# Kernel tuning notes

Measured on AMD Instinct MI355X. Metric: run time of the kernel, lower is better.

The kernel has to match this reference:

```python
import jax, jax.numpy as jnp
import numpy as np

EMBED_DIM = 1024
N_HEADS = 16
HEAD_DIM = EMBED_DIM // N_HEADS
SEQ_LEN = 4096


def setup_inputs() -> dict:
    key = jax.random.key(0)
    k1, k2 = jax.random.split(key)
    x = jax.random.normal(k1, (SEQ_LEN, EMBED_DIM), dtype=jnp.float32)
    # Linear params (lecun-normal-ish scale)
    W_qkv = jax.random.normal(k2, (EMBED_DIM, 3 * EMBED_DIM), dtype=jnp.float32) / np.sqrt(EMBED_DIM)
    b_qkv = jnp.zeros((3 * EMBED_DIM,), dtype=jnp.float32)
    return {"x": x, "W_qkv": W_qkv, "b_qkv": b_qkv}


def reference(x, W_qkv, b_qkv):
    T = x.shape[0]
    # Fused QKV projection: [T, 3*E]
    qkv = x @ W_qkv + b_qkv
    q, k, v = jnp.split(qkv, 3, axis=-1)
    # [T, N, H]
    q = q.reshape(T, N_HEADS, HEAD_DIM)
    k = k.reshape(T, N_HEADS, HEAD_DIM)
    v = v.reshape(T, N_HEADS, HEAD_DIM)
    # Standard SDPA (module does NOT pass is_causal, so full attention)
    scale = 1.0 / np.sqrt(HEAD_DIM).astype(np.float32)
    logits = jnp.einsum("qnh,knh->nqk", q, k) * scale  # [N, T, T]
    attn = jax.nn.softmax(logits, axis=-1)
    y = jnp.einsum("nqk,knh->qnh", attn, v)  # [T, N, H]
    return y
```

## Files before the change

### kernel.cpp

```cpp
#include <hip/hip_runtime.h>

#define T_SEQ 4096
#define EMB   1024
#define NH    16
#define HD    64
#define N3    3072

#define SCL2 0.18033688011112042f

using u16 = unsigned short;
using u32 = unsigned int;
typedef __bf16 bf16x8 __attribute__((ext_vector_type(8)));
typedef float  f32x4  __attribute__((ext_vector_type(4)));
typedef float  f32x16 __attribute__((ext_vector_type(16)));
typedef u16    u16x8  __attribute__((ext_vector_type(8)));

#if __has_builtin(__builtin_amdgcn_exp2f)
#define EXP2(x) __builtin_amdgcn_exp2f(x)
#else
#define EXP2(x) exp2f(x)
#endif

__device__ inline u16 f2bf(float f) {
    union { float f; unsigned u; } v; v.f = f;
    unsigned u = v.u;
    u += 0x7FFFu + ((u >> 16) & 1u);
    return (u16)(u >> 16);
}

__global__ void convert_x_kernel(const float* __restrict__ x, u16* __restrict__ xb) {
    int i = (blockIdx.x * 256 + threadIdx.x) * 8;
    float4 a = *(const float4*)(x + i);
    float4 b = *(const float4*)(x + i + 4);
    u16x8 o;
    o[0] = f2bf(a.x); o[1] = f2bf(a.y); o[2] = f2bf(a.z); o[3] = f2bf(a.w);
    o[4] = f2bf(b.x); o[5] = f2bf(b.y); o[6] = f2bf(b.z); o[7] = f2bf(b.w);
    *(u16x8*)(xb + i) = o;
}

__global__ void transpose_w_kernel(const float* __restrict__ W, u16* __restrict__ Wt) {
    __shared__ float tile[64][72];
    int n0 = blockIdx.x * 64, k0 = blockIdx.y * 64;
    float qs = (n0 < 1024) ? SCL2 : 1.0f;
    int t = threadIdx.x;
#pragma unroll
    for (int p = 0; p < 16; ++p) {
        int idx = p * 256 + t;
        int r = idx >> 6, c = idx & 63;
        tile[r][c] = W[(k0 + r) * N3 + n0 + c];
    }
    __syncthreads();
    int c2 = t >> 2;
    int kg = (t & 3) * 16;
    u16x8 o0, o1;
#pragma unroll
    for (int j = 0; j < 8; ++j) o0[j] = f2bf(tile[kg + j][c2] * qs);
#pragma unroll
    for (int j = 0; j < 8; ++j) o1[j] = f2bf(tile[kg + 8 + j][c2] * qs);
    u16* dst = Wt + (n0 + c2) * EMB + k0 + kg;
    *(u16x8*)dst = o0;
    *(u16x8*)(dst + 8) = o1;
}

__global__ __launch_bounds__(256) void gemm_qkv_kernel(const u16* __restrict__ xb,
                                                       const u16* __restrict__ Wt,
                                                       const float* __restrict__ bias,
                                                       u16* __restrict__ qkv) {
    __shared__ __align__(16) u16 Alds[128 * 64];
    __shared__ __align__(16) u16 Blds[128 * 64];
    int tid = threadIdx.x;
    int lane = tid & 63, wave = tid >> 6;
    int wm = wave >> 1, wn = wave & 1;
    int m0 = blockIdx.y * 128, n0 = blockIdx.x * 128;
    int lr = lane & 15, lg = lane >> 4;

    f32x4 acc[4][4] = {};

    for (int kt = 0; kt < 16; ++kt) {
        int kbase = kt * 64;
#pragma unroll
        for (int p = 0; p < 4; ++p) {
            int g = p * 256 + tid;
            int row = g >> 3;
            int cg = (g & 7) << 3;
            int sg = (((cg >> 3) ^ (row & 7)) << 3);
            u16x8 va = *(const u16x8*)(xb + (m0 + row) * EMB + kbase + cg);
            *(u16x8*)&Alds[row * 64 + sg] = va;
            u16x8 vb = *(const u16x8*)(Wt + (n0 + row) * EMB + kbase + cg);
            *(u16x8*)&Blds[row * 64 + sg] = vb;
        }
        __syncthreads();
#pragma unroll
        for (int ks = 0; ks < 2; ++ks) {
            bf16x8 af[4], bf[4];
#pragma unroll
            for (int mi = 0; mi < 4; ++mi) {
                int row = wm * 64 + mi * 16 + lr;
                int sg = ((ks * 4 + lg) ^ (row & 7)) << 3;
                af[mi] = *(const bf16x8*)&Alds[row * 64 + sg];
            }
#pragma unroll
            for (int ni = 0; ni < 4; ++ni) {
                int row = wn * 64 + ni * 16 + lr;
                int sg = ((ks * 4 + lg) ^ (row & 7)) << 3;
                bf[ni] = *(const bf16x8*)&Blds[row * 64 + sg];
            }
#pragma unroll
            for (int mi = 0; mi < 4; ++mi)
#pragma unroll
                for (int ni = 0; ni < 4; ++ni)
                    acc[mi][ni] = __builtin_amdgcn_mfma_f32_16x16x32_bf16(af[mi], bf[ni], acc[mi][ni], 0, 0, 0);
        }
        __syncthreads();
    }
#pragma unroll
    for (int ni = 0; ni < 4; ++ni) {
        int n = n0 + wn * 64 + ni * 16 + lr;
        float bv = bias[n];
        if (n < 1024) bv *= SCL2;
#pragma unroll
        for (int mi = 0; mi < 4; ++mi) {
            int mrow = m0 + wm * 64 + mi * 16 + lg * 4;
#pragma unroll
            for (int r = 0; r < 4; ++r)
                qkv[(mrow + r) * N3 + n] = f2bf(acc[mi][ni][r] + bv);
        }
    }
}

__global__ void transpose_v_kernel(const u16* __restrict__ qkv, u16* __restrict__ Vt) {
    __shared__ u16 tile[64][72];
    int c0 = blockIdx.x * 64;
    int t0 = blockIdx.y * 64;
    int t = threadIdx.x;
#pragma unroll
    for (int p = 0; p < 16; ++p) {
        int idx = p * 256 + t;
        int r = idx >> 6, c = idx & 63;
        tile[r][c] = qkv[(t0 + r) * N3 + 2048 + c0 + c];
    }
    __syncthreads();
    int c2 = t >> 2;
    int kg = (t & 3) * 16;
    u16x8 o0, o1;
#pragma unroll
    for (int j = 0; j < 8; ++j) o0[j] = tile[kg + j][c2];
#pragma unroll
    for (int j = 0; j < 8; ++j) o1[j] = tile[kg + 8 + j][c2];
    u16* dst = Vt + (c0 + c2) * T_SEQ + t0 + kg;
    *(u16x8*)dst = o0;
    *(u16x8*)(dst + 8) = o1;
}

__device__ inline u32 cvtpk(float lo, float hi) {
    u32 r;
    asm("v_cvt_pk_bf16_f32 %0, %1, %2" : "=v"(r) : "v"(lo), "v"(hi));
    return r;
}

__device__ inline bf16x8 mk8(u32 w0, u32 w1, u32 w2, u32 w3) {
    union { u32 w[4]; bf16x8 v; } u;
    u.w[0] = w0; u.w[1] = w1; u.w[2] = w2; u.w[3] = w3;
    return u.v;
}

__device__ inline float vsum16(f32x16 v) {
    float a0 = v[0] + v[1],  a1 = v[2] + v[3];
    float a2 = v[4] + v[5],  a3 = v[6] + v[7];
    float a4 = v[8] + v[9],  a5 = v[10] + v[11];
    float a6 = v[12] + v[13], a7 = v[14] + v[15];
    float b0 = a0 + a1, b1 = a2 + a3, b2 = a4 + a5, b3 = a6 + a7;
    return (b0 + b1) + (b2 + b3);
}

__device__ inline void pack2(f32x16 p, int hi, bf16x8& fe, bf16x8& fo) {
    u32 a0 = cvtpk(p[0], p[1]),   a1 = cvtpk(p[2], p[3]);
    u32 a2 = cvtpk(p[4], p[5]),   a3 = cvtpk(p[6], p[7]);
    u32 b0 = cvtpk(p[8], p[9]),   b1 = cvtpk(p[10], p[11]);
    u32 b2 = cvtpk(p[12], p[13]), b3 = cvtpk(p[14], p[15]);
    u32 xa0 = (u32)__shfl_xor((int)a0, 32), xa1 = (u32)__shfl_xor((int)a1, 32);
    u32 xa2 = (u32)__shfl_xor((int)a2, 32), xa3 = (u32)__shfl_xor((int)a3, 32);
    u32 xb0 = (u32)__shfl_xor((int)b0, 32), xb1 = (u32)__shfl_xor((int)b1, 32);
    u32 xb2 = (u32)__shfl_xor((int)b2, 32), xb3 = (u32)__shfl_xor((int)b3, 32);
    fe = hi ? mk8(xa2, xa3, a2, a3) : mk8(a0, a1, xa0, xa1);
    fo = hi ? mk8(xb2, xb3, b2, b3) : mk8(b0, b1, xb0, xb1);
}

#define KVROW 72

__global__ __launch_bounds__(512, 4) void attn_kernel(const u16* __restrict__ qkv,
                                                      const u16* __restrict__ Vt,
                                                      float* __restrict__ out) {
    __shared__ __align__(16) char smem[73728];

    int tid = threadIdx.x, lane = tid & 63, wave = tid >> 6;
    int ql = lane & 31, hi = lane >> 5;
    int g = tid >> 8;
    int wq = wave & 3;
    int tid2 = tid & 255;
    int h = blockIdx.y;
    int q0 = blockIdx.x * 128;

    char* base = smem + g * 36864;
    u16* K0 = (u16*)base;
    u16* V0 = (u16*)(base + 9216);
    u16* K1 = (u16*)(base + 18432);
    u16* V1 = (u16*)(base + 27648);

    bf16x8 qf[4];
    {
        const u16* qp = qkv + (size_t)(q0 + wq * 32 + ql) * N3 + h * HD;
#pragma unroll
        for (int c = 0; c < 4; ++c)
            qf[c] = *(const bf16x8*)(qp + c * 16 + hi * 8);
    }

    f32x16 acc0 = {}, acc1 = {};
    float lrun = 0.f;

    int srow0 = tid2 >> 3, spg = tid2 & 7;
    int srow1 = srow0 + 32;
    const u16* kptr = qkv + (size_t)(g * 2048) * N3 + EMB + h * HD;
    const u16* vptr = Vt + (size_t)(h * HD) * T_SEQ + g * 2048;
    int woff0 = srow0 * KVROW + spg * 8;
    int woff1 = srow1 * KVROW + spg * 8;

    u16x8 kst0 = *(const u16x8*)(kptr + (size_t)srow0 * N3 + spg * 8);
    u16x8 kst1 = *(const u16x8*)(kptr + (size_t)srow1 * N3 + spg * 8);
    u16x8 vst0 = *(const u16x8*)(vptr + (size_t)srow0 * T_SEQ + spg * 8);
    u16x8 vst1 = *(const u16x8*)(vptr + (size_t)srow1 * T_SEQ + spg * 8);

    int koff = ql * KVROW + hi * 8;

    for (int t = 0; t < 32; ++t) {
        u16* Kl = (t & 1) ? K1 : K0;
        u16* Vl = (t & 1) ? V1 : V0;
        *(u16x8*)&Kl[woff0] = kst0;
        *(u16x8*)&Kl[woff1] = kst1;
        *(u16x8*)&Vl[woff0] = vst0;
        *(u16x8*)&Vl[woff1] = vst1;
        if (t < 31) {
            const u16* kb = kptr + (size_t)(t + 1) * 64 * N3;
            const u16* vb = vptr + (t + 1) * 64;
            kst0 = *(const u16x8*)(kb + (size_t)srow0 * N3 + spg * 8);
            kst1 = *(const u16x8*)(kb + (size_t)srow1 * N3 + spg * 8);
            vst0 = *(const u16x8*)(vb + (size_t)srow0 * T_SEQ + spg * 8);
            vst1 = *(const u16x8*)(vb + (size_t)srow1 * T_SEQ + spg * 8);
        }
        __syncthreads();

        f32x16 s0 = {}, s1 = {};
#pragma unroll
        for (int c = 0; c < 4; ++c) {
            bf16x8 kf = *(const bf16x8*)&Kl[koff + c * 16];
            s0 = __builtin_amdgcn_mfma_f32_32x32x16_bf16(kf, qf[c], s0, 0, 0, 0);
        }
#pragma unroll
        for (int c = 0; c < 4; ++c) {
            bf16x8 kf = *(const bf16x8*)&Kl[koff + 32 * KVROW + c * 16];
            s1 = __builtin_amdgcn_mfma_f32_32x32x16_bf16(kf, qf[c], s1, 0, 0, 0);
        }

#pragma unroll
        for (int r = 0; r < 16; ++r) s0[r] = EXP2(s0[r]);
#pragma unroll
        for (int r = 0; r < 16; ++r) s1[r] = EXP2(s1[r]);

        {
            float ss = vsum16(s0) + vsum16(s1);
            ss += __shfl_xor(ss, 32);
            lrun += ss;
        }

        bf16x8 pa0, pa1, pa2, pa3;
        pack2(s0, hi, pa0, pa1);
        pack2(s1, hi, pa2, pa3);

#pragma unroll
        for (int c = 0; c < 4; ++c) {
            bf16x8 pb = (c == 0) ? pa0 : (c == 1) ? pa1 : (c == 2) ? pa2 : pa3;
            bf16x8 vf0 = *(const bf16x8*)&Vl[koff + c * 16];
            acc0 = __builtin_amdgcn_mfma_f32_32x32x16_bf16(vf0, pb, acc0, 0, 0, 0);
            bf16x8 vf1 = *(const bf16x8*)&Vl[koff + 32 * KVROW + c * 16];
            acc1 = __builtin_amdgcn_mfma_f32_32x32x16_bf16(vf1, pb, acc1, 0, 0, 0);
        }
    }

    __syncthreads();

    float* Xb = (float*)(smem + 36864);
    float* lX = Xb + 4 * 32 * 68;

    if (g == 1) {
        float* ob = Xb + wq * (32 * 68);
#pragma unroll
        for (int gg = 0; gg < 4; ++gg) {
            f32x4 w0 = { acc0[4 * gg], acc0[4 * gg + 1], acc0[4 * gg + 2], acc0[4 * gg + 3] };
            *(f32x4*)&ob[ql * 68 + 8 * gg + 4 * hi] = w0;
            f32x4 w1 = { acc1[4 * gg], acc1[4 * gg + 1], acc1[4 * gg + 2], acc1[4 * gg + 3] };
            *(f32x4*)&ob[ql * 68 + 32 + 8 * gg + 4 * hi] = w1;
        }
        if (hi == 0) lX[wq * 32 + ql] = lrun;
    }
    __syncthreads();

    if (g == 0) {
        float* ob = Xb + wq * (32 * 68);
        float inv = 1.0f / (lrun + lX[wq * 32 + ql]);
        float* tb = (float*)smem + wq * (32 * 68);
#pragma unroll
        for (int gg = 0; gg < 4; ++gg) {
            f32x4 x0 = *(const f32x4*)&ob[ql * 68 + 8 * gg + 4 * hi];
            f32x4 w0 = { (acc0[4 * gg] + x0[0]) * inv, (acc0[4 * gg + 1] + x0[1]) * inv,
                         (acc0[4 * gg + 2] + x0[2]) * inv, (acc0[4 * gg + 3] + x0[3]) * inv };
            *(f32x4*)&tb[ql * 68 + 8 * gg + 4 * hi] = w0;
            f32x4 x1 = *(const f32x4*)&ob[ql * 68 + 32 + 8 * gg + 4 * hi];
            f32x4 w1 = { (acc1[4 * gg] + x1[0]) * inv, (acc1[4 * gg + 1] + x1[1]) * inv,
                         (acc1[4 * gg + 2] + x1[2]) * inv, (acc1[4 * gg + 3] + x1[3]) * inv };
            *(f32x4*)&tb[ql * 68 + 32 + 8 * gg + 4 * hi] = w1;
        }
    }
    __syncthreads();

    if (g == 0) {
        float* tb = (float*)smem + wq * (32 * 68);
#pragma unroll
        for (int qq = 0; qq < 8; ++qq) {
            int q = qq * 4 + (lane >> 4);
            int d4 = (lane & 15) * 4;
            f32x4 v = *(const f32x4*)&tb[q * 68 + d4];
            *(f32x4*)&out[(size_t)(q0 + wq * 32 + q) * EMB + h * HD + d4] = v;
        }
    }
}

extern "C" void kernel_launch(void* const* d_in, const int* in_sizes, int n_in,
                              void* d_out, int out_size, void* d_ws, size_t ws_size,
                              hipStream_t stream) {
    (void)in_sizes; (void)n_in; (void)out_size; (void)ws_size;
    const float* x = (const float*)d_in[0];
    const float* W = (const float*)d_in[1];
    const float* b = (const float*)d_in[2];
    float* out = (float*)d_out;

    u16* xb  = (u16*)d_ws;
    u16* Wt  = xb  + (size_t)T_SEQ * EMB;
    u16* qkv = Wt  + (size_t)N3 * EMB;
    u16* Vt  = qkv + (size_t)T_SEQ * N3;

    convert_x_kernel<<<(T_SEQ * EMB) / (256 * 8), 256, 0, stream>>>(x, xb);
    transpose_w_kernel<<<dim3(N3 / 64, EMB / 64), 256, 0, stream>>>(W, Wt);
    gemm_qkv_kernel<<<dim3(N3 / 128, T_SEQ / 128), 256, 0, stream>>>(xb, Wt, b, qkv);
    transpose_v_kernel<<<dim3(EMB / 64, T_SEQ / 64), 256, 0, stream>>>(qkv, Vt);
    attn_kernel<<<dim3(T_SEQ / 128, NH), 512, 0, stream>>>(qkv, Vt, out);
}
```

Before: 155.9 us.

## Give each attention wave two 32-row query tiles, halving block threads

The attention block drops from 512 to 256 threads. Each wave now processes 64 query rows (two 32-row tiles) against every K/V fragment it reads from shared memory, so each LDS fragment load feeds two MFMAs. Each thread stages four K/V rows per tile instead of two. This cuts LDS read traffic per FLOP and the number of waves sharing a block, at the cost of roughly double the accumulator and score registers per wave, which may lower occupancy or cause spills. The epilogue is updated to merge 64-row halves between the two key-split groups.

```diff
diff --git a/kernel.cpp b/kernel.cpp
--- a/kernel.cpp
+++ b/kernel.cpp
@@ -188,16 +188,16 @@
 
 #define KVROW 72
 
-__global__ __launch_bounds__(512, 4) void attn_kernel(const u16* __restrict__ qkv,
+__global__ __launch_bounds__(256, 2) void attn_kernel(const u16* __restrict__ qkv,
                                                       const u16* __restrict__ Vt,
                                                       float* __restrict__ out) {
     __shared__ __align__(16) char smem[73728];
 
     int tid = threadIdx.x, lane = tid & 63, wave = tid >> 6;
     int ql = lane & 31, hi = lane >> 5;
-    int g = tid >> 8;
-    int wq = wave & 3;
-    int tid2 = tid & 255;
+    int g = wave >> 1;
+    int wq = wave & 1;
+    int tid2 = tid & 127;
     int h = blockIdx.y;
     int q0 = blockIdx.x * 128;
 
@@ -207,129 +207,165 @@
     u16* K1 = (u16*)(base + 18432);
     u16* V1 = (u16*)(base + 27648);
 
-    bf16x8 qf[4];
+    bf16x8 qfA[4], qfB[4];
     {
-        const u16* qp = qkv + (size_t)(q0 + wq * 32 + ql) * N3 + h * HD;
-#pragma unroll
-        for (int c = 0; c < 4; ++c)
-            qf[c] = *(const bf16x8*)(qp + c * 16 + hi * 8);
-    }
-
-    f32x16 acc0 = {}, acc1 = {};
-    float lrun = 0.f;
-
-    int srow0 = tid2 >> 3, spg = tid2 & 7;
-    int srow1 = srow0 + 32;
+        const u16* qpA = qkv + (size_t)(q0 + wq * 64 + ql) * N3 + h * HD;
+        const u16* qpB = qpA + (size_t)32 * N3;
+#pragma unroll
+        for (int c = 0; c < 4; ++c) {
+            qfA[c] = *(const bf16x8*)(qpA + c * 16 + hi * 8);
+            qfB[c] = *(const bf16x8*)(qpB + c * 16 + hi * 8);
+        }
+    }
+
+    f32x16 accA0 = {}, accA1 = {}, accB0 = {}, accB1 = {};
+    float lrA = 0.f, lrB = 0.f;
+
+    int srow = (tid2 >> 3) & 15, spg = tid2 & 7;
     const u16* kptr = qkv + (size_t)(g * 2048) * N3 + EMB + h * HD;
     const u16* vptr = Vt + (size_t)(h * HD) * T_SEQ + g * 2048;
-    int woff0 = srow0 * KVROW + spg * 8;
-    int woff1 = srow1 * KVROW + spg * 8;
-
-    u16x8 kst0 = *(const u16x8*)(kptr + (size_t)srow0 * N3 + spg * 8);
-    u16x8 kst1 = *(const u16x8*)(kptr + (size_t)srow1 * N3 + spg * 8);
-    u16x8 vst0 = *(const u16x8*)(vptr + (size_t)srow0 * T_SEQ + spg * 8);
-    u16x8 vst1 = *(const u16x8*)(vptr + (size_t)srow1 * T_SEQ + spg * 8);
+
+    u16x8 kstg[4], vstg[4];
+#pragma unroll
+    for (int j = 0; j < 4; ++j) {
+        kstg[j] = *(const u16x8*)(kptr + (size_t)(srow + 16 * j) * N3 + spg * 8);
+        vstg[j] = *(const u16x8*)(vptr + (size_t)(srow + 16 * j) * T_SEQ + spg * 8);
+    }
 
     int koff = ql * KVROW + hi * 8;
 
     for (int t = 0; t < 32; ++t) {
         u16* Kl = (t & 1) ? K1 : K0;
         u16* Vl = (t & 1) ? V1 : V0;
-        *(u16x8*)&Kl[woff0] = kst0;
-        *(u16x8*)&Kl[woff1] = kst1;
-        *(u16x8*)&Vl[woff0] = vst0;
-        *(u16x8*)&Vl[woff1] = vst1;
+#pragma unroll
+        for (int j = 0; j < 4; ++j) {
+            *(u16x8*)&Kl[(srow + 16 * j) * KVROW + spg * 8] = kstg[j];
+            *(u16x8*)&Vl[(srow + 16 * j) * KVROW + spg * 8] = vstg[j];
+        }
         if (t < 31) {
             const u16* kb = kptr + (size_t)(t + 1) * 64 * N3;
             const u16* vb = vptr + (t + 1) * 64;
-            kst0 = *(const u16x8*)(kb + (size_t)srow0 * N3 + spg * 8);
-            kst1 = *(const u16x8*)(kb + (size_t)srow1 * N3 + spg * 8);
-            vst0 = *(const u16x8*)(vb + (size_t)srow0 * T_SEQ + spg * 8);
-            vst1 = *(const u16x8*)(vb + (size_t)srow1 * T_SEQ + spg * 8);
+#pragma unroll
+            for (int j = 0; j < 4; ++j) {
+                kstg[j] = *(const u16x8*)(kb + (size_t)(srow + 16 * j) * N3 + spg * 8);
+                vstg[j] = *(const u16x8*)(vb + (size_t)(srow + 16 * j) * T_SEQ + spg * 8);
+            }
         }
         __syncthreads();
 
-        f32x16 s0 = {}, s1 = {};
+        f32x16 sA0 = {}, sA1 = {}, sB0 = {}, sB1 = {};
 #pragma unroll
         for (int c = 0; c < 4; ++c) {
             bf16x8 kf = *(const bf16x8*)&Kl[koff + c * 16];
-            s0 = __builtin_amdgcn_mfma_f32_32x32x16_bf16(kf, qf[c], s0, 0, 0, 0);
+            sA0 = __builtin_amdgcn_mfma_f32_32x32x16_bf16(kf, qfA[c], sA0, 0, 0, 0);
+            sB0 = __builtin_amdgcn_mfma_f32_32x32x16_bf16(kf, qfB[c], sB0, 0, 0, 0);
         }
 #pragma unroll
         for (int c = 0; c < 4; ++c) {
             bf16x8 kf = *(const bf16x8*)&Kl[koff + 32 * KVROW + c * 16];
-            s1 = __builtin_amdgcn_mfma_f32_32x32x16_bf16(kf, qf[c], s1, 0, 0, 0);
-        }
-
-#pragma unroll
-        for (int r = 0; r < 16; ++r) s0[r] = EXP2(s0[r]);
-#pragma unroll
-        for (int r = 0; r < 16; ++r) s1[r] = EXP2(s1[r]);
+            sA1 = __builtin_amdgcn_mfma_f32_32x32x16_bf16(kf, qfA[c], sA1, 0, 0, 0);
+            sB1 = __builtin_amdgcn_mfma_f32_32x32x16_bf16(kf, qfB[c], sB1, 0, 0, 0);
+        }
+
+#pragma unroll
+        for (int r = 0; r < 16; ++r) sA0[r] = EXP2(sA0[r]);
+#pragma unroll
+        for (int r = 0; r < 16; ++r) sA1[r] = EXP2(sA1[r]);
+#pragma unroll
+        for (int r = 0; r < 16; ++r) sB0[r] = EXP2(sB0[r]);
+#pragma unroll
+        for (int r = 0; r < 16; ++r) sB1[r] = EXP2(sB1[r]);
 
         {
-            float ss = vsum16(s0) + vsum16(s1);
-            ss += __shfl_xor(ss, 32);
-            lrun += ss;
-        }
-
-        bf16x8 pa0, pa1, pa2, pa3;
-        pack2(s0, hi, pa0, pa1);
-        pack2(s1, hi, pa2, pa3);
+            float sa = vsum16(sA0) + vsum16(sA1);
+            sa += __shfl_xor(sa, 32);
+            lrA += sa;
+            float sb = vsum16(sB0) + vsum16(sB1);
+            sb += __shfl_xor(sb, 32);
+            lrB += sb;
+        }
+
+        bf16x8 paA0, paA1, paA2, paA3, paB0, paB1, paB2, paB3;
+        pack2(sA0, hi, paA0, paA1);
+        pack2(sA1, hi, paA2, paA3);
+        pack2(sB0, hi, paB0, paB1);
+        pack2(sB1, hi, paB2, paB3);
 
 #pragma unroll
         for (int c = 0; c < 4; ++c) {
-            bf16x8 pb = (c == 0) ? pa0 : (c == 1) ? pa1 : (c == 2) ? pa2 : pa3;
+            bf16x8 pbA = (c == 0) ? paA0 : (c == 1) ? paA1 : (c == 2) ? paA2 : paA3;
+            bf16x8 pbB = (c == 0) ? paB0 : (c == 1) ? paB1 : (c == 2) ? paB2 : paB3;
             bf16x8 vf0 = *(const bf16x8*)&Vl[koff + c * 16];
-            acc0 = __builtin_amdgcn_mfma_f32_32x32x16_bf16(vf0, pb, acc0, 0, 0, 0);
+            accA0 = __builtin_amdgcn_mfma_f32_32x32x16_bf16(vf0, pbA, accA0, 0, 0, 0);
+            accB0 = __builtin_amdgcn_mfma_f32_32x32x16_bf16(vf0, pbB, accB0, 0, 0, 0);
             bf16x8 vf1 = *(const bf16x8*)&Vl[koff + 32 * KVROW + c * 16];
-            acc1 = __builtin_amdgcn_mfma_f32_32x32x16_bf16(vf1, pb, acc1, 0, 0, 0);
+            accA1 = __builtin_amdgcn_mfma_f32_32x32x16_bf16(vf1, pbA, accA1, 0, 0, 0);
+            accB1 = __builtin_amdgcn_mfma_f32_32x32x16_bf16(vf1, pbB, accB1, 0, 0, 0);
         }
     }
 
     __syncthreads();
 
     float* Xb = (float*)(smem + 36864);
-    float* lX = Xb + 4 * 32 * 68;
+    float* lX = Xb + 2 * 64 * 68;
 
     if (g == 1) {
-        float* ob = Xb + wq * (32 * 68);
+        float* ob = Xb + wq * (64 * 68);
 #pragma unroll
         for (int gg = 0; gg < 4; ++gg) {
-            f32x4 w0 = { acc0[4 * gg], acc0[4 * gg + 1], acc0[4 * gg + 2], acc0[4 * gg + 3] };
-            *(f32x4*)&ob[ql * 68 + 8 * gg + 4 * hi] = w0;
-            f32x4 w1 = { acc1[4 * gg], acc1[4 * gg + 1], acc1[4 * gg + 2], acc1[4 * gg + 3] };
-            *(f32x4*)&ob[ql * 68 + 32 + 8 * gg + 4 * hi] = w1;
-        }
-        if (hi == 0) lX[wq * 32 + ql] = lrun;
+            int d = 8 * gg + 4 * hi;
+            f32x4 a0 = { accA0[4 * gg], accA0[4 * gg + 1], accA0[4 * gg + 2], accA0[4 * gg + 3] };
+            *(f32x4*)&ob[ql * 68 + d] = a0;
+            f32x4 a1 = { accA1[4 * gg], accA1[4 * gg + 1], accA1[4 * gg + 2], accA1[4 * gg + 3] };
+            *(f32x4*)&ob[ql * 68 + 32 + d] = a1;
+            f32x4 b0 = { accB0[4 * gg], accB0[4 * gg + 1], accB0[4 * gg + 2], accB0[4 * gg + 3] };
+            *(f32x4*)&ob[(32 + ql) * 68 + d] = b0;
+            f32x4 b1 = { accB1[4 * gg], accB1[4 * gg + 1], accB1[4 * gg + 2], accB1[4 * gg + 3] };
+            *(f32x4*)&ob[(32 + ql) * 68 + 32 + d] = b1;
+        }
+        if (hi == 0) {
+            lX[wq * 64 + ql] = lrA;
+            lX[wq * 64 + 32 + ql] = lrB;
+        }
     }
     __syncthreads();
 
     if (g == 0) {
-        float* ob = Xb + wq * (32 * 68);
-        float inv = 1.0f / (lrun + lX[wq * 32 + ql]);
-        float* tb = (float*)smem + wq * (32 * 68);
+        float* ob = Xb + wq * (64 * 68);
+        float invA = 1.0f / (lrA + lX[wq * 64 + ql]);
+        float invB = 1.0f / (lrB + lX[wq * 64 + 32 + ql]);
+        float* tb = (float*)smem + wq * (64 * 68);
 #pragma unroll
         for (int gg = 0; gg < 4; ++gg) {
-            f32x4 x0 = *(const f32x4*)&ob[ql * 68 + 8 * gg + 4 * hi];
-            f32x4 w0 = { (acc0[4 * gg] + x0[0]) * inv, (acc0[4 * gg + 1] + x0[1]) * inv,
-                         (acc0[4 * gg + 2] + x0[2]) * inv, (acc0[4 * gg + 3] + x0[3]) * inv };
-            *(f32x4*)&tb[ql * 68 + 8 * gg + 4 * hi] = w0;
-            f32x4 x1 = *(const f32x4*)&ob[ql * 68 + 32 + 8 * gg + 4 * hi];
-            f32x4 w1 = { (acc1[4 * gg] + x1[0]) * inv, (acc1[4 * gg + 1] + x1[1]) * inv,
-                         (acc1[4 * gg + 2] + x1[2]) * inv, (acc1[4 * gg + 3] + x1[3]) * inv };
-            *(f32x4*)&tb[ql * 68 + 32 + 8 * gg + 4 * hi] = w1;
+            int d = 8 * gg + 4 * hi;
+            f32x4 xa0 = *(const f32x4*)&ob[ql * 68 + d];
+            f32x4 wa0 = { (accA0[4 * gg] + xa0[0]) * invA, (accA0[4 * gg + 1] + xa0[1]) * invA,
+                          (accA0[4 * gg + 2] + xa0[2]) * invA, (accA0[4 * gg + 3] + xa0[3]) * invA };
+            *(f32x4*)&tb[ql * 68 + d] = wa0;
+            f32x4 xa1 = *(const f32x4*)&ob[ql * 68 + 32 + d];
+            f32x4 wa1 = { (accA1[4 * gg] + xa1[0]) * invA, (accA1[4 * gg + 1] + xa1[1]) * invA,
+                          (accA1[4 * gg + 2] + xa1[2]) * invA, (accA1[4 * gg + 3] + xa1[3]) * invA };
+            *(f32x4*)&tb[ql * 68 + 32 + d] = wa1;
+            f32x4 xb0 = *(const f32x4*)&ob[(32 + ql) * 68 + d];
+            f32x4 wb0 = { (accB0[4 * gg] + xb0[0]) * invB, (accB0[4 * gg + 1] + xb0[1]) * invB,
+                          (accB0[4 * gg + 2] + xb0[2]) * invB, (accB0[4 * gg + 3] + xb0[3]) * invB };
+            *(f32x4*)&tb[(32 + ql) * 68 + d] = wb0;
+            f32x4 xb1 = *(const f32x4*)&ob[(32 + ql) * 68 + 32 + d];
+            f32x4 wb1 = { (accB1[4 * gg] + xb1[0]) * invB, (accB1[4 * gg + 1] + xb1[1]) * invB,
+                          (accB1[4 * gg + 2] + xb1[2]) * invB, (accB1[4 * gg + 3] + xb1[3]) * invB };
+            *(f32x4*)&tb[(32 + ql) * 68 + 32 + d] = wb1;
         }
     }
     __syncthreads();
 
     if (g == 0) {
-        float* tb = (float*)smem + wq * (32 * 68);
-#pragma unroll
-        for (int qq = 0; qq < 8; ++qq) {
+        float* tb = (float*)smem + wq * (64 * 68);
+#pragma unroll
+        for (int qq = 0; qq < 16; ++qq) {
             int q = qq * 4 + (lane >> 4);
             int d4 = (lane & 15) * 4;
             f32x4 v = *(const f32x4*)&tb[q * 68 + d4];
-            *(f32x4*)&out[(size_t)(q0 + wq * 32 + q) * EMB + h * HD + d4] = v;
+            *(f32x4*)&out[(size_t)(q0 + wq * 64 + q) * EMB + h * HD + d4] = v;
         }
     }
 }
@@ -352,5 +388,5 @@
     transpose_w_kernel<<<dim3(N3 / 64, EMB / 64), 256, 0, stream>>>(W, Wt);
     gemm_qkv_kernel<<<dim3(N3 / 128, T_SEQ / 128), 256, 0, stream>>>(xb, Wt, b, qkv);
     transpose_v_kernel<<<dim3(EMB / 64, T_SEQ / 64), 256, 0, stream>>>(qkv, Vt);
-    attn_kernel<<<dim3(T_SEQ / 128, NH), 512, 0, stream>>>(qkv, Vt, out);
-}
+    attn_kernel<<<dim3(T_SEQ / 128, NH), 256, 0, stream>>>(qkv, Vt, out);
+}
```

New measurement: 162.5 us. 4.3% more time.
